# Optimization experiments

Hardware: AMD Instinct MI355X
Metric: run time of the kernel (lower is better)

The kernel has to match this reference:

```python
import jax, jax.numpy as jnp
import numpy as np

H = 64
N_PERSON = 200000
N_MOVIE = 100000
E_ACTED = 1600000
E_DIRECTED = 200000
E_WWW = 3200000
N_LAYERS = 2


def setup_inputs() -> dict:
    key = jax.random.key(0)
    ks = jax.random.split(key, 24)
    s = 1.0 / np.sqrt(H)
    inp = {
        "x_person": jax.random.normal(ks[0], (N_PERSON, H), jnp.float32),
        "x_movie": jax.random.normal(ks[1], (N_MOVIE, H), jnp.float32),
        "acted_src": jax.random.randint(ks[2], (E_ACTED,), 0, N_PERSON, jnp.int32),
        "acted_dst": jax.random.randint(ks[3], (E_ACTED,), 0, N_MOVIE, jnp.int32),
        "directed_src": jax.random.randint(ks[4], (E_DIRECTED,), 0, N_PERSON, jnp.int32),
        "directed_dst": jax.random.randint(ks[5], (E_DIRECTED,), 0, N_MOVIE, jnp.int32),
        "www_src": jax.random.randint(ks[6], (E_WWW,), 0, N_PERSON, jnp.int32),
        "www_dst": jax.random.randint(ks[7], (E_WWW,), 0, N_PERSON, jnp.int32),
        # per-relation SAGEConv params, stacked over the 2 layers
        "Wl_acted": jax.random.normal(ks[8], (N_LAYERS, H, H), jnp.float32) * s,
        "bl_acted": jnp.zeros((N_LAYERS, H), jnp.float32),
        "Wr_acted": jax.random.normal(ks[9], (N_LAYERS, H, H), jnp.float32) * s,
        "Wl_directed": jax.random.normal(ks[10], (N_LAYERS, H, H), jnp.float32) * s,
        "bl_directed": jnp.zeros((N_LAYERS, H), jnp.float32),
        "Wr_directed": jax.random.normal(ks[11], (N_LAYERS, H, H), jnp.float32) * s,
        "Wl_www": jax.random.normal(ks[12], (N_LAYERS, H, H), jnp.float32) * s,
        "bl_www": jnp.zeros((N_LAYERS, H), jnp.float32),
        "Wr_www": jax.random.normal(ks[13], (N_LAYERS, H, H), jnp.float32) * s,
        "lin_W": jax.random.normal(ks[14], (1, H), jnp.float32) * s,
        "lin_b": jnp.zeros((1,), jnp.float32),
    }
    return inp


def sage_conv(x_src, x_dst, src, dst, Wl, bl, Wr, n_dst):
    # PyG SAGEConv: mean-aggregate source feats at dst, then lin_l(agg) + lin_r(x_dst)
    agg = jax.ops.segment_sum(x_src[src], dst, num_segments=n_dst)  # [n_dst, H_in]
    cnt = jax.ops.segment_sum(jnp.ones((src.shape[0],), x_src.dtype), dst, num_segments=n_dst)
    mean = agg / jnp.maximum(cnt, 1.0)[:, None]
    return mean @ Wl.T + bl + x_dst @ Wr.T


def reference(x_person, x_movie, acted_src, acted_dst, directed_src, directed_dst,
              www_src, www_dst, Wl_acted, bl_acted, Wr_acted,
              Wl_directed, bl_directed, Wr_directed,
              Wl_www, bl_www, Wr_www, lin_W, lin_b):
    x_p, x_m = x_person, x_movie
    for l in range(N_LAYERS):
        # HeteroConv(aggr='sum'): movie receives sum of acted_in and directed convs
        out_m = sage_conv(x_p, x_m, acted_src, acted_dst,
                          Wl_acted[l], bl_acted[l], Wr_acted[l], N_MOVIE)
        out_m = out_m + sage_conv(x_p, x_m, directed_src, directed_dst,
                                  Wl_directed[l], bl_directed[l], Wr_directed[l], N_MOVIE)
        out_p = sage_conv(x_p, x_p, www_src, www_dst,
                          Wl_www[l], bl_www[l], Wr_www[l], N_PERSON)
        x_m = jax.nn.relu(out_m)
        x_p = jax.nn.relu(out_p)
    return (x_m @ lin_W.T + lin_b).squeeze(-1)  # [N_MOVIE]
```

## Files before the change

### kernel.cpp

```cpp
#include <hip/hip_runtime.h>

#define H 64
#define N_PERSON 200000
#define N_MOVIE 100000
#define E_ACTED 1600000
#define E_DIRECTED 200000
#define E_WWW 3200000
#define E_TOTAL (E_ACTED + E_DIRECTED + E_WWW)

#define SH 11
#define NBIN 2048
#define CH 16384

typedef __attribute__((ext_vector_type(8))) short bf16x8;
typedef __attribute__((ext_vector_type(4))) float f32x4;

static __device__ __forceinline__ ushort f2bf(float f) {
  uint u = __float_as_uint(f);
  uint r = (u + 0x7FFFu + ((u >> 16) & 1u)) >> 16;
  return (ushort)r;
}
static __device__ __forceinline__ float bflo(uint u) { return __uint_as_float(u << 16); }
static __device__ __forceinline__ float bfhiq(uint u) { return __uint_as_float(u); }
static __device__ __forceinline__ uint packbf(float lo, float hi) {
  return (uint)f2bf(lo) | ((uint)f2bf(hi) << 16);
}


struct RelP {
  const int* src; const int* dst; int* off;
  int E, N, nblk, nbuk, blkbase, bukbase, cbase, ebase;
};


static __global__ __launch_bounds__(256) void cast_all_k(const float* __restrict__ i0,
                                                         ushort* __restrict__ o0, int n0,
                                                         const float* __restrict__ i1,
                                                         ushort* __restrict__ o1, int n1) {
  int i = blockIdx.x * 256 + threadIdx.x;
  int stride = gridDim.x * 256;
  int nt = n0 + n1;
  for (; i < nt; i += stride) {
    const float4* in; ushort4* out; int idx;
    if (i < n0) { in = (const float4*)i0; out = (ushort4*)o0; idx = i; }
    else { in = (const float4*)i1; out = (ushort4*)o1; idx = i - n0; }
    float4 v = in[idx];
    ushort4 o;
    o.x = f2bf(v.x); o.y = f2bf(v.y); o.z = f2bf(v.z); o.w = f2bf(v.w);
    out[idx] = o;
  }
}


static __global__ __launch_bounds__(1024) void scan_block_k(const int* __restrict__ in, int n,
                                                            int* __restrict__ out,
                                                            int* __restrict__ partials) {
  __shared__ int sm[1024];
  int tid = threadIdx.x;
  int gid = blockIdx.x * 1024 + tid;
  int v = (gid < n) ? in[gid] : 0;
  sm[tid] = v;
  __syncthreads();
  for (int d = 1; d < 1024; d <<= 1) {
    int t = (tid >= d) ? sm[tid - d] : 0;
    __syncthreads();
    if (tid >= d) sm[tid] += t;
    __syncthreads();
  }
  if (gid < n) out[gid] = sm[tid] - v;
  if (tid == 1023 && partials) partials[blockIdx.x] = sm[1023];
}

static __global__ __launch_bounds__(1024) void add_off_k(int* __restrict__ off, int n,
                                                         const int* __restrict__ parts, int total) {
  int gid = blockIdx.x * 1024 + threadIdx.x;
  if (gid < n) off[gid] += parts[gid >> 10];
  else if (gid == n) off[gid] = total;
}


static __global__ __launch_bounds__(256) void part_count_all_k(RelP a, RelP b, RelP c,
                                                               int* __restrict__ counts) {
  __shared__ int hist[128];
  int blk = blockIdx.x, t = threadIdx.x;
  RelP r = (blk >= c.blkbase) ? c : (blk >= b.blkbase) ? b : a;
  int lb = blk - r.blkbase;
  for (int i = t; i < r.nbuk; i += 256) hist[i] = 0;
  __syncthreads();
  int e0 = lb * CH, e1 = min(e0 + CH, r.E);
  for (int e = e0 + t; e < e1; e += 256) atomicAdd(&hist[r.dst[e] >> SH], 1);
  __syncthreads();
  for (int i = t; i < r.nbuk; i += 256) counts[r.cbase + i * r.nblk + lb] = hist[i];
}

static __global__ __launch_bounds__(256) void part_scatter_all_k(RelP a, RelP b, RelP c,
                                                                 const int* __restrict__ off_bb,
                                                                 int* __restrict__ pairs) {
  __shared__ int cur[128];
  int blk = blockIdx.x, t = threadIdx.x;
  RelP r = (blk >= c.blkbase) ? c : (blk >= b.blkbase) ? b : a;
  int lb = blk - r.blkbase;
  for (int i = t; i < r.nbuk; i += 256) cur[i] = off_bb[r.cbase + i * r.nblk + lb];
  __syncthreads();
  int e0 = lb * CH, e1 = min(e0 + CH, r.E);
  int e = e0 + t;
  for (; e + 256 < e1; e += 512) {
    int d0 = r.dst[e], s0 = r.src[e];
    int d1 = r.dst[e + 256], s1 = r.src[e + 256];
    int p0 = atomicAdd(&cur[d0 >> SH], 1);
    int p1 = atomicAdd(&cur[d1 >> SH], 1);
    pairs[p0] = ((d0 & (NBIN - 1)) << 18) | s0;
    pairs[p1] = ((d1 & (NBIN - 1)) << 18) | s1;
  }
  if (e < e1) {
    int d0 = r.dst[e], s0 = r.src[e];
    int p0 = atomicAdd(&cur[d0 >> SH], 1);
    pairs[p0] = ((d0 & (NBIN - 1)) << 18) | s0;
  }
}

static __global__ __launch_bounds__(1024) void fine_sort_all_k(RelP a, RelP b, RelP c,
                                                               const int* __restrict__ off_bb,
                                                               const int* __restrict__ pairs,
                                                               int* __restrict__ csr) {
  __shared__ int hist[NBIN];
  __shared__ int sc[NBIN];
  int bb = blockIdx.x, t = threadIdx.x;
  RelP r = (bb >= c.bukbase) ? c : (bb >= b.bukbase) ? b : a;
  int bkt = bb - r.bukbase;
  int bstart = off_bb[r.cbase + bkt * r.nblk];
  int bend = (bkt + 1 < r.nbuk) ? off_bb[r.cbase + (bkt + 1) * r.nblk] : (r.ebase + r.E);
  int base = bkt << SH;
  hist[t] = 0; hist[t + 1024] = 0;
  __syncthreads();
  for (int e = bstart + t; e < bend; e += 1024) atomicAdd(&hist[((uint)pairs[e]) >> 18], 1);
  __syncthreads();
  sc[t] = hist[t]; sc[t + 1024] = hist[t + 1024];
  __syncthreads();
  for (int d = 1; d < NBIN; d <<= 1) {
    int v0 = (t >= d) ? sc[t - d] : 0;
    int v1 = (t + 1024 >= d) ? sc[t + 1024 - d] : 0;
    __syncthreads();
    sc[t] += v0; sc[t + 1024] += v1;
    __syncthreads();
  }
  int ex0 = sc[t] - hist[t];
  int ex1 = sc[t + 1024] - hist[t + 1024];
  if (base + t < r.N) r.off[base + t] = bstart + ex0;
  if (base + t + 1024 < r.N) r.off[base + t + 1024] = bstart + ex1;
  if (bkt == r.nbuk - 1 && t == 0) r.off[r.N] = r.ebase + r.E;
  hist[t] = ex0; hist[t + 1024] = ex1;
  __syncthreads();
  for (int e = bstart + t; e < bend; e += 1024) {
    int p = pairs[e];
    int pos = bstart + atomicAdd(&hist[((uint)p) >> 18], 1);
    csr[pos] = p & 0x3FFFF;
  }
}


struct PullT { const ushort* xsrc; const int* off; ushort* mean; int n; int blkbase; };

#define ACC8(u)                                  \
  do {                                           \
    a0 += bflo((u).x); a1 += bfhiq((u).x);       \
    a2 += bflo((u).y); a3 += bfhiq((u).y);       \
    a4 += bflo((u).z); a5 += bfhiq((u).z);       \
    a6 += bflo((u).w); a7 += bfhiq((u).w);       \
  } while (0)

static __global__ __launch_bounds__(256) void pull_all_k(PullT t0, PullT t1, PullT t2,
                                                         const int* __restrict__ csr) {
  int blk = blockIdx.x;
  PullT tk;
  if (t2.n > 0 && blk >= t2.blkbase) tk = t2;
  else if (blk >= t1.blkbase) tk = t1;
  else tk = t0;
  int lane = threadIdx.x & 63;
  int g = lane >> 3;
  int fo = lane & 7;
  int d = ((blk - tk.blkbase) * 4 + (threadIdx.x >> 6)) * 8 + g;
  bool dok = d < tk.n;
  int dd = dok ? d : (tk.n - 1);
  int e0 = tk.off[dd];
  int e1 = tk.off[dd + 1];
  int cnt = dok ? (e1 - e0) : 0;
  int mx = cnt;
  mx = max(mx, __shfl_xor(mx, 8, 64));
  mx = max(mx, __shfl_xor(mx, 16, 64));
  mx = max(mx, __shfl_xor(mx, 32, 64));

  const ushort* __restrict__ xrow = tk.xsrc + fo * 8;
  float a0 = 0.f, a1 = 0.f, a2 = 0.f, a3 = 0.f, a4 = 0.f, a5 = 0.f, a6 = 0.f, a7 = 0.f;

  int i = 0;
  for (; i + 2 <= mx; i += 2) {
    if (i + 1 < cnt) {
      int s0 = csr[e0 + i];
      int s1 = csr[e0 + i + 1];
      uint4 u0 = *(const uint4*)(xrow + (size_t)s0 * 64);
      uint4 u1 = *(const uint4*)(xrow + (size_t)s1 * 64);
      ACC8(u0); ACC8(u1);
    } else if (i < cnt) {
      int s0 = csr[e0 + i];
      uint4 u0 = *(const uint4*)(xrow + (size_t)s0 * 64);
      ACC8(u0);
    }
  }
  if (i < mx && i < cnt) {
    int s0 = csr[e0 + i];
    uint4 u0 = *(const uint4*)(xrow + (size_t)s0 * 64);
    ACC8(u0);
  }

  if (dok) {
    float inv = 1.0f / fmaxf((float)cnt, 1.0f);
    uint4 o;
    o.x = packbf(a0 * inv, a1 * inv);
    o.y = packbf(a2 * inv, a3 * inv);
    o.z = packbf(a4 * inv, a5 * inv);
    o.w = packbf(a6 * inv, a7 * inv);
    *(uint4*)(tk.mean + (size_t)d * 64 + fo * 8) = o;
  }
}


struct GemmT {
  const ushort *A0, *A1, *A2;
  const float *W0, *W1, *W2, *Wadd, *b0, *b1;
  ushort* outB;
  const float *projW, *projb;
  float* projOut;
  int M, nsrc, blkbase;
};

static __global__ __launch_bounds__(256) void gemm_all_k(GemmT g0, GemmT g1) {
  GemmT g = (g1.M > 0 && (int)blockIdx.x >= g1.blkbase) ? g1 : g0;
  __shared__ ushort Wt[3][64][72];
  const int t = threadIdx.x;
  const int w = t >> 6;
  const int l = t & 63;
  const int lr = l & 15;
  const int lk = l >> 4;
  const int m0 = ((int)blockIdx.x - g.blkbase) * 256;

  auto stageW = [&](const float* W, int s, const float* Wa) {
#pragma unroll
    for (int i = 0; i < 8; ++i) {
      int dp = t + i * 256;
      int j = dp >> 5;
      int kk = (dp & 31) * 2;
      float2 wv = *(const float2*)(W + j * 64 + kk);
      if (Wa) {
        float2 av = *(const float2*)(Wa + j * 64 + kk);
        wv.x += av.x; wv.y += av.y;
      }
      *(uint*)&Wt[s][j][kk] = packbf(wv.x, wv.y);
    }
  };
  stageW(g.W0, 0, nullptr);
  stageW(g.W1, 1, g.nsrc == 2 ? g.Wadd : nullptr);
  if (g.nsrc > 2) stageW(g.W2, 2, g.Wadd);
  __syncthreads();

  f32x4 acc[4][4];
#pragma unroll
  for (int mt = 0; mt < 4; ++mt)
#pragma unroll
    for (int jt = 0; jt < 4; ++jt) acc[mt][jt] = (f32x4){0.f, 0.f, 0.f, 0.f};

  auto doSrc = [&](const ushort* A, int s) {
    bf16x8 aF[4][2];
#pragma unroll
    for (int mt = 0; mt < 4; ++mt) {
      int m = m0 + w * 64 + mt * 16 + lr;
      const ushort* ap = A + (size_t)(m < g.M ? m : 0) * 64 + lk * 8;
      aF[mt][0] = *(const bf16x8*)(ap);
      aF[mt][1] = *(const bf16x8*)(ap + 32);
    }
#pragma unroll
    for (int jt = 0; jt < 4; ++jt) {
#pragma unroll
      for (int k0 = 0; k0 < 2; ++k0) {
        bf16x8 bF = *(const bf16x8*)&Wt[s][jt * 16 + lr][k0 * 32 + lk * 8];
#pragma unroll
        for (int mt = 0; mt < 4; ++mt)
          acc[mt][jt] =
              __builtin_amdgcn_mfma_f32_16x16x32_bf16(bF, aF[mt][k0], acc[mt][jt], 0, 0, 0);
      }
    }
  };
  doSrc(g.A0, 0);
  doSrc(g.A1, 1);
  if (g.nsrc > 2) doSrc(g.A2, 2);

  f32x4 bv[4];
#pragma unroll
  for (int jt = 0; jt < 4; ++jt) {
    f32x4 b = (f32x4){0.f, 0.f, 0.f, 0.f};
    if (g.b0) b += *(const f32x4*)(g.b0 + jt * 16 + lk * 4);
    if (g.b1) b += *(const f32x4*)(g.b1 + jt * 16 + lk * 4);
    bv[jt] = b;
  }

  if (g.projOut) {
    f32x4 pw[4];
#pragma unroll
    for (int jt = 0; jt < 4; ++jt) pw[jt] = *(const f32x4*)(g.projW + jt * 16 + lk * 4);
    float pb = g.projb[0];
#pragma unroll
    for (int mt = 0; mt < 4; ++mt) {
      float p = 0.f;
#pragma unroll
      for (int jt = 0; jt < 4; ++jt) {
        f32x4 o = acc[mt][jt] + bv[jt];
#pragma unroll
        for (int q = 0; q < 4; ++q) p += fmaxf(o[q], 0.f) * pw[jt][q];
      }
      p += __shfl_xor(p, 16, 64);
      p += __shfl_xor(p, 32, 64);
      int m = m0 + w * 64 + mt * 16 + lr;
      if (lk == 0 && m < g.M) g.projOut[m] = p + pb;
    }
  } else {
#pragma unroll
    for (int mt = 0; mt < 4; ++mt) {
      int m = m0 + w * 64 + mt * 16 + lr;
      if (m < g.M) {
        ushort* row = g.outB + (size_t)m * 64 + lk * 4;
#pragma unroll
        for (int jt = 0; jt < 4; ++jt) {
          f32x4 o = acc[mt][jt] + bv[jt];
          uint2 pk;
          pk.x = packbf(fmaxf(o[0], 0.f), fmaxf(o[1], 0.f));
          pk.y = packbf(fmaxf(o[2], 0.f), fmaxf(o[3], 0.f));
          *(uint2*)(row + jt * 16) = pk;
        }
      }
    }
  }
}


extern "C" void kernel_launch(void* const* d_in, const int* in_sizes, int n_in, void* d_out,
                              int out_size, void* d_ws, size_t ws_size, hipStream_t stream) {
  const float* x_person = (const float*)d_in[0];
  const float* x_movie = (const float*)d_in[1];
  const int* acted_src = (const int*)d_in[2];
  const int* acted_dst = (const int*)d_in[3];
  const int* directed_src = (const int*)d_in[4];
  const int* directed_dst = (const int*)d_in[5];
  const int* www_src = (const int*)d_in[6];
  const int* www_dst = (const int*)d_in[7];
  const float* Wl_acted = (const float*)d_in[8];
  const float* bl_acted = (const float*)d_in[9];
  const float* Wr_acted = (const float*)d_in[10];
  const float* Wl_directed = (const float*)d_in[11];
  const float* bl_directed = (const float*)d_in[12];
  const float* Wr_directed = (const float*)d_in[13];
  const float* Wl_www = (const float*)d_in[14];
  const float* bl_www = (const float*)d_in[15];
  const float* Wr_www = (const float*)d_in[16];
  const float* lin_W = (const float*)d_in[17];
  const float* lin_b = (const float*)d_in[18];
  float* out = (float*)d_out;
  (void)in_sizes; (void)n_in; (void)out_size; (void)ws_size;

  char* base = (char*)d_ws;
  size_t pos = 0;
  auto carve = [&](size_t b) -> void* {
    void* r = base + pos;
    pos += (b + 255) & ~(size_t)255;
    return r;
  };
  int* off_a = (int*)carve((N_MOVIE + 1) * sizeof(int));
  int* off_d = (int*)carve((N_MOVIE + 1) * sizeof(int));
  int* off_w = (int*)carve((N_PERSON + 1) * sizeof(int));
  int* parts = (int*)carve(1024 * sizeof(int));
  int* csr_all = (int*)carve((size_t)E_TOTAL * sizeof(int));
  int* pairs = (int*)carve((size_t)E_TOTAL * sizeof(int));
  ushort* xpbf = (ushort*)carve((size_t)N_PERSON * H * sizeof(ushort));
  ushort* xmbf = (ushort*)carve((size_t)N_MOVIE * H * sizeof(ushort));
  ushort* xp0bf = (ushort*)carve((size_t)N_PERSON * H * sizeof(ushort));
  ushort* xm0bf = (ushort*)carve((size_t)N_MOVIE * H * sizeof(ushort));
  ushort* meanAbf = (ushort*)carve((size_t)N_MOVIE * H * sizeof(ushort));
  ushort* meanDbf = (ushort*)carve((size_t)N_MOVIE * H * sizeof(ushort));
  ushort* meanWbf = (ushort*)carve((size_t)N_PERSON * H * sizeof(ushort));

  RelP rA, rD, rW;
  rA.src = acted_src;  rA.dst = acted_dst;  rA.off = off_a;
  rA.E = E_ACTED;      rA.N = N_MOVIE;
  rA.nblk = (E_ACTED + CH - 1) / CH;      rA.nbuk = (N_MOVIE + NBIN - 1) >> SH;
  rD.src = directed_src; rD.dst = directed_dst; rD.off = off_d;
  rD.E = E_DIRECTED;     rD.N = N_MOVIE;
  rD.nblk = (E_DIRECTED + CH - 1) / CH;   rD.nbuk = (N_MOVIE + NBIN - 1) >> SH;
  rW.src = www_src;    rW.dst = www_dst;  rW.off = off_w;
  rW.E = E_WWW;        rW.N = N_PERSON;
  rW.nblk = (E_WWW + CH - 1) / CH;        rW.nbuk = (N_PERSON + NBIN - 1) >> SH;
  rA.blkbase = 0;                 rD.blkbase = rA.nblk;           rW.blkbase = rA.nblk + rD.nblk;
  rA.bukbase = 0;                 rD.bukbase = rA.nbuk;           rW.bukbase = rA.nbuk + rD.nbuk;
  rA.cbase = 0;                   rD.cbase = rA.nbuk * rA.nblk;
  rW.cbase = rD.cbase + rD.nbuk * rD.nblk;
  rA.ebase = 0;                   rD.ebase = E_ACTED;             rW.ebase = E_ACTED + E_DIRECTED;
  const int n_total = rW.cbase + rW.nbuk * rW.nblk;
  const int nblk_total = rW.blkbase + rW.nblk;
  const int nbuk_total = rW.bukbase + rW.nbuk;

  int* counts = (int*)carve((size_t)n_total * sizeof(int));
  int* off_bb = (int*)carve((size_t)(n_total + 1) * sizeof(int));

  part_count_all_k<<<nblk_total, 256, 0, stream>>>(rA, rD, rW, counts);
  int nb = (n_total + 1023) / 1024;
  scan_block_k<<<nb, 1024, 0, stream>>>(counts, n_total, off_bb, parts);
  scan_block_k<<<1, 1024, 0, stream>>>(parts, nb, parts, nullptr);
  add_off_k<<<(n_total + 1 + 1023) / 1024, 1024, 0, stream>>>(off_bb, n_total, parts, E_TOTAL);
  part_scatter_all_k<<<nblk_total, 256, 0, stream>>>(rA, rD, rW, off_bb, pairs);
  fine_sort_all_k<<<nbuk_total, 1024, 0, stream>>>(rA, rD, rW, off_bb, pairs, csr_all);

  cast_all_k<<<2048, 256, 0, stream>>>(x_person, xpbf, N_PERSON * H / 4, x_movie, xmbf,
                                       N_MOVIE * H / 4);

  const int nbA = (N_MOVIE + 31) / 32, nbD = (N_MOVIE + 31) / 32, nbW = (N_PERSON + 31) / 32;
  const int gmM = (N_MOVIE + 255) / 256, gmP = (N_PERSON + 255) / 256;

  {
    PullT pA = {xpbf, off_a, meanAbf, N_MOVIE, 0};
    PullT pD = {xpbf, off_d, meanDbf, N_MOVIE, nbA};
    PullT pW = {xpbf, off_w, meanWbf, N_PERSON, nbA + nbD};
    pull_all_k<<<nbA + nbD + nbW, 256, 0, stream>>>(pA, pD, pW, csr_all);
  }
  {
    GemmT gM = {meanAbf, meanDbf, xmbf,
                Wl_acted, Wl_directed, Wr_acted, Wr_directed, bl_acted, bl_directed,
                xm0bf, nullptr, nullptr, nullptr, N_MOVIE, 3, 0};
    GemmT gP = {meanWbf, xpbf, nullptr,
                Wl_www, Wr_www, nullptr, nullptr, bl_www, nullptr,
                xp0bf, nullptr, nullptr, nullptr, N_PERSON, 2, gmM};
    gemm_all_k<<<gmM + gmP, 256, 0, stream>>>(gM, gP);
  }
  {
    PullT pA = {xp0bf, off_a, meanAbf, N_MOVIE, 0};
    PullT pD = {xp0bf, off_d, meanDbf, N_MOVIE, nbA};
    PullT pZ = {nullptr, nullptr, nullptr, 0, 0};
    pull_all_k<<<nbA + nbD, 256, 0, stream>>>(pA, pD, pZ, csr_all);
  }
  {
    GemmT gM = {meanAbf, meanDbf, xm0bf,
                Wl_acted + 4096, Wl_directed + 4096, Wr_acted + 4096, Wr_directed + 4096,
                bl_acted + 64, bl_directed + 64,
                nullptr, lin_W, lin_b, out, N_MOVIE, 3, 0};
    GemmT gZ = {nullptr, nullptr, nullptr, nullptr, nullptr, nullptr, nullptr, nullptr, nullptr,
                nullptr, nullptr, nullptr, nullptr, 0, 0, 0};
    gemm_all_k<<<gmM, 256, 0, stream>>>(gM, gZ);
  }
}
```

Before: 344.3 us.

## Fuse cast into count kernel, single-block scan, wave-shuffle scan in fine sort

Result: slower. 352.9 us (+2.5%).

```diff
diff --git a/kernel.cpp b/kernel.cpp
--- a/kernel.cpp
+++ b/kernel.cpp
@@ -33,56 +33,29 @@
 };
 
 
-static __global__ __launch_bounds__(256) void cast_all_k(const float* __restrict__ i0,
-                                                         ushort* __restrict__ o0, int n0,
-                                                         const float* __restrict__ i1,
-                                                         ushort* __restrict__ o1, int n1) {
-  int i = blockIdx.x * 256 + threadIdx.x;
-  int stride = gridDim.x * 256;
-  int nt = n0 + n1;
-  for (; i < nt; i += stride) {
-    const float4* in; ushort4* out; int idx;
-    if (i < n0) { in = (const float4*)i0; out = (ushort4*)o0; idx = i; }
-    else { in = (const float4*)i1; out = (ushort4*)o1; idx = i - n0; }
-    float4 v = in[idx];
-    ushort4 o;
-    o.x = f2bf(v.x); o.y = f2bf(v.y); o.z = f2bf(v.z); o.w = f2bf(v.w);
-    out[idx] = o;
-  }
-}
-
-
-static __global__ __launch_bounds__(1024) void scan_block_k(const int* __restrict__ in, int n,
-                                                            int* __restrict__ out,
-                                                            int* __restrict__ partials) {
-  __shared__ int sm[1024];
-  int tid = threadIdx.x;
-  int gid = blockIdx.x * 1024 + tid;
-  int v = (gid < n) ? in[gid] : 0;
-  sm[tid] = v;
-  __syncthreads();
-  for (int d = 1; d < 1024; d <<= 1) {
-    int t = (tid >= d) ? sm[tid - d] : 0;
-    __syncthreads();
-    if (tid >= d) sm[tid] += t;
-    __syncthreads();
-  }
-  if (gid < n) out[gid] = sm[tid] - v;
-  if (tid == 1023 && partials) partials[blockIdx.x] = sm[1023];
-}
-
-static __global__ __launch_bounds__(1024) void add_off_k(int* __restrict__ off, int n,
-                                                         const int* __restrict__ parts, int total) {
-  int gid = blockIdx.x * 1024 + threadIdx.x;
-  if (gid < n) off[gid] += parts[gid >> 10];
-  else if (gid == n) off[gid] = total;
-}
-
-
-static __global__ __launch_bounds__(256) void part_count_all_k(RelP a, RelP b, RelP c,
-                                                               int* __restrict__ counts) {
+static __global__ __launch_bounds__(256) void count_cast_k(RelP a, RelP b, RelP c,
+                                                           int* __restrict__ counts, int castbase,
+                                                           const float* __restrict__ i0,
+                                                           ushort* __restrict__ o0, int n0,
+                                                           const float* __restrict__ i1,
+                                                           ushort* __restrict__ o1, int n1) {
+  int blk = blockIdx.x, t = threadIdx.x;
+  if (blk >= castbase) {
+    int i = (blk - castbase) * 256 + t;
+    int stride = 2048 * 256;
+    int nt = n0 + n1;
+    for (; i < nt; i += stride) {
+      const float4* in; ushort4* out; int idx;
+      if (i < n0) { in = (const float4*)i0; out = (ushort4*)o0; idx = i; }
+      else { in = (const float4*)i1; out = (ushort4*)o1; idx = i - n0; }
+      float4 v = in[idx];
+      ushort4 o;
+      o.x = f2bf(v.x); o.y = f2bf(v.y); o.z = f2bf(v.z); o.w = f2bf(v.w);
+      out[idx] = o;
+    }
+    return;
+  }
   __shared__ int hist[128];
-  int blk = blockIdx.x, t = threadIdx.x;
   RelP r = (blk >= c.blkbase) ? c : (blk >= b.blkbase) ? b : a;
   int lb = blk - r.blkbase;
   for (int i = t; i < r.nbuk; i += 256) hist[i] = 0;
@@ -92,6 +65,34 @@
   __syncthreads();
   for (int i = t; i < r.nbuk; i += 256) counts[r.cbase + i * r.nblk + lb] = hist[i];
 }
+
+
+static __global__ __launch_bounds__(1024) void scan_one_k(const int* __restrict__ in, int n,
+                                                          int* __restrict__ out, int total) {
+  __shared__ int wsum[16];
+  int t = threadIdx.x;
+  int C = (n + 1023) / 1024;
+  int i0 = t * C, i1 = min(i0 + C, n);
+  int s = 0;
+  for (int i = i0; i < i1; ++i) s += in[i];
+  int lane = t & 63, w = t >> 6;
+  int incl = s;
+  for (int d = 1; d < 64; d <<= 1) {
+    int v = __shfl_up(incl, d, 64);
+    if (lane >= d) incl += v;
+  }
+  if (lane == 63) wsum[w] = incl;
+  __syncthreads();
+  if (t == 0) {
+    int acc = 0;
+    for (int i = 0; i < 16; ++i) { int v = wsum[i]; wsum[i] = acc; acc += v; }
+  }
+  __syncthreads();
+  int run = wsum[w] + (incl - s);
+  for (int i = i0; i < i1; ++i) { int v = in[i]; out[i] = run; run += v; }
+  if (t == 0) out[n] = total;
+}
+
 
 static __global__ __launch_bounds__(256) void part_scatter_all_k(RelP a, RelP b, RelP c,
                                                                  const int* __restrict__ off_bb,
@@ -119,37 +120,45 @@
   }
 }
 
+
 static __global__ __launch_bounds__(1024) void fine_sort_all_k(RelP a, RelP b, RelP c,
                                                                const int* __restrict__ off_bb,
                                                                const int* __restrict__ pairs,
                                                                int* __restrict__ csr) {
   __shared__ int hist[NBIN];
-  __shared__ int sc[NBIN];
+  __shared__ int wsum[16];
   int bb = blockIdx.x, t = threadIdx.x;
   RelP r = (bb >= c.bukbase) ? c : (bb >= b.bukbase) ? b : a;
   int bkt = bb - r.bukbase;
   int bstart = off_bb[r.cbase + bkt * r.nblk];
   int bend = (bkt + 1 < r.nbuk) ? off_bb[r.cbase + (bkt + 1) * r.nblk] : (r.ebase + r.E);
   int base = bkt << SH;
-  hist[t] = 0; hist[t + 1024] = 0;
+  int b0 = t * 2, b1 = t * 2 + 1;
+  hist[b0] = 0; hist[b1] = 0;
   __syncthreads();
   for (int e = bstart + t; e < bend; e += 1024) atomicAdd(&hist[((uint)pairs[e]) >> 18], 1);
   __syncthreads();
-  sc[t] = hist[t]; sc[t + 1024] = hist[t + 1024];
-  __syncthreads();
-  for (int d = 1; d < NBIN; d <<= 1) {
-    int v0 = (t >= d) ? sc[t - d] : 0;
-    int v1 = (t + 1024 >= d) ? sc[t + 1024 - d] : 0;
-    __syncthreads();
-    sc[t] += v0; sc[t + 1024] += v1;
-    __syncthreads();
-  }
-  int ex0 = sc[t] - hist[t];
-  int ex1 = sc[t + 1024] - hist[t + 1024];
-  if (base + t < r.N) r.off[base + t] = bstart + ex0;
-  if (base + t + 1024 < r.N) r.off[base + t + 1024] = bstart + ex1;
+  int h0 = hist[b0], h1 = hist[b1];
+  int s = h0 + h1;
+  int lane = t & 63, w = t >> 6;
+  int incl = s;
+  for (int d = 1; d < 64; d <<= 1) {
+    int v = __shfl_up(incl, d, 64);
+    if (lane >= d) incl += v;
+  }
+  if (lane == 63) wsum[w] = incl;
+  __syncthreads();
+  if (t == 0) {
+    int acc = 0;
+    for (int i = 0; i < 16; ++i) { int v = wsum[i]; wsum[i] = acc; acc += v; }
+  }
+  __syncthreads();
+  int excl = wsum[w] + (incl - s);
+  int ex0 = excl, ex1 = excl + h0;
+  if (base + b0 < r.N) r.off[base + b0] = bstart + ex0;
+  if (base + b1 < r.N) r.off[base + b1] = bstart + ex1;
   if (bkt == r.nbuk - 1 && t == 0) r.off[r.N] = r.ebase + r.E;
-  hist[t] = ex0; hist[t + 1024] = ex1;
+  hist[b0] = ex0; hist[b1] = ex1;
   __syncthreads();
   for (int e = bstart + t; e < bend; e += 1024) {
     int p = pairs[e];
@@ -376,7 +385,6 @@
   int* off_a = (int*)carve((N_MOVIE + 1) * sizeof(int));
   int* off_d = (int*)carve((N_MOVIE + 1) * sizeof(int));
   int* off_w = (int*)carve((N_PERSON + 1) * sizeof(int));
-  int* parts = (int*)carve(1024 * sizeof(int));
   int* csr_all = (int*)carve((size_t)E_TOTAL * sizeof(int));
   int* pairs = (int*)carve((size_t)E_TOTAL * sizeof(int));
   ushort* xpbf = (ushort*)carve((size_t)N_PERSON * H * sizeof(ushort));
@@ -409,16 +417,12 @@
   int* counts = (int*)carve((size_t)n_total * sizeof(int));
   int* off_bb = (int*)carve((size_t)(n_total + 1) * sizeof(int));
 
-  part_count_all_k<<<nblk_total, 256, 0, stream>>>(rA, rD, rW, counts);
-  int nb = (n_total + 1023) / 1024;
-  scan_block_k<<<nb, 1024, 0, stream>>>(counts, n_total, off_bb, parts);
-  scan_block_k<<<1, 1024, 0, stream>>>(parts, nb, parts, nullptr);
-  add_off_k<<<(n_total + 1 + 1023) / 1024, 1024, 0, stream>>>(off_bb, n_total, parts, E_TOTAL);
+  count_cast_k<<<nblk_total + 2048, 256, 0, stream>>>(rA, rD, rW, counts, nblk_total, x_person,
+                                                      xpbf, N_PERSON * H / 4, x_movie, xmbf,
+                                                      N_MOVIE * H / 4);
+  scan_one_k<<<1, 1024, 0, stream>>>(counts, n_total, off_bb, E_TOTAL);
   part_scatter_all_k<<<nblk_total, 256, 0, stream>>>(rA, rD, rW, off_bb, pairs);
   fine_sort_all_k<<<nbuk_total, 1024, 0, stream>>>(rA, rD, rW, off_bb, pairs, csr_all);
-
-  cast_all_k<<<2048, 256, 0, stream>>>(x_person, xpbf, N_PERSON * H / 4, x_movie, xmbf,
-                                       N_MOVIE * H / 4);
 
   const int nbA = (N_MOVIE + 31) / 32, nbD = (N_MOVIE + 31) / 32, nbW = (N_PERSON + 31) / 32;
   const int gmM = (N_MOVIE + 255) / 256, gmP = (N_PERSON + 255) / 256;
```
